# Kernel optimization log

Measured on AMD Instinct MI355X. Metric: run time of the kernel, lower is better.

## Reference

```python
import jax, jax.numpy as jnp
import numpy as np

HEADS = 4
DIM_HEAD = 128
HIDDEN = HEADS * DIM_HEAD  # 512
DIM = 256
EMBED = 256


def mish(x):
    return x * jnp.tanh(jax.nn.softplus(x))


def setup_inputs() -> dict:
    key = jax.random.key(0)
    k = jax.random.split(key, 7)
    b, a, f, t = 64, 8, DIM, 256
    x = jax.random.normal(k[0], (b, a, f, t), dtype=jnp.float32)
    time = jax.random.normal(k[1], (b, a, EMBED), dtype=jnp.float32)
    # to_qkv: Conv2d(dim, 3*hidden, 1, bias=False) -> weight [3*hidden, dim]
    w_qkv = jax.random.normal(k[2], (3 * HIDDEN, DIM), dtype=jnp.float32) * (1.0 / np.sqrt(DIM))
    # time_mlp: Mish -> Linear(embed, 3*hidden)
    w_time = jax.random.normal(k[3], (3 * HIDDEN, EMBED), dtype=jnp.float32) * (1.0 / np.sqrt(EMBED))
    b_time = jax.random.normal(k[4], (3 * HIDDEN,), dtype=jnp.float32) * 0.01
    # to_out: Conv2d(hidden, dim, 1) with bias
    w_out = jax.random.normal(k[5], (DIM, HIDDEN), dtype=jnp.float32) * (1.0 / np.sqrt(HIDDEN))
    b_out = jax.random.normal(k[6], (DIM,), dtype=jnp.float32) * 0.01
    return {"x": x, "time": time, "w_qkv": w_qkv, "w_time": w_time,
            "b_time": b_time, "w_out": w_out, "b_out": b_out}


def reference(x, time, w_qkv, w_time, b_time, w_out, b_out):
    b, a, f, t = x.shape
    heads, c = HEADS, DIM_HEAD
    # x: b a f t -> b f a t (channels-first for 1x1 conv)
    xp = jnp.transpose(x, (0, 2, 1, 3))  # [b, f, a, t]
    # 1x1 conv == channel GEMM
    qkv = jnp.einsum('of,bfat->boat', w_qkv, xp)  # [b, 3*hidden, a, t]
    # time MLP: Mish -> Linear; bias broadcast over t
    temb = mish(time) @ w_time.T + b_time          # [b, a, 3*hidden]
    temb = jnp.transpose(temb, (0, 2, 1))[..., None]  # [b, 3*hidden, a, 1]
    qkv = qkv + temb
    # 'b (qkv heads c) h w -> qkv (b h) heads c w' with h=a, w=t
    qkv = qkv.reshape(b, 3, heads, c, a, t)
    qkv = jnp.transpose(qkv, (1, 0, 4, 2, 3, 5)).reshape(3, b * a, heads, c, t)
    q, k, v = qkv[0], qkv[1], qkv[2]  # each [(b a), heads, c, t]
    k = jax.nn.softmax(k, axis=-1)
    # linear attention: context over keys/values, then apply to q
    context = jnp.einsum('bhdn,bhen->bhde', k, v)   # [(b a), heads, c, c]
    out = jnp.einsum('bhde,bhdn->bhen', context, q)  # [(b a), heads, c, t]
    # '(b h) heads c w -> b (heads c) h w'
    out = out.reshape(b, a, heads * c, t)
    out = jnp.transpose(out, (0, 2, 1, 3))  # [b, hidden, a, t]
    out = jnp.einsum('of,bfat->boat', w_out, out) + b_out[None, :, None, None]
    # b f a t -> b a f t
    return jnp.transpose(out, (0, 2, 1, 3))
```

## Files before the change

kernel.cpp:

```cpp
#include <hip/hip_runtime.h>

typedef __bf16 bf16;
typedef __bf16 bf16x4 __attribute__((ext_vector_type(4)));
typedef __bf16 bf16x8 __attribute__((ext_vector_type(8)));
typedef float  f32x4  __attribute__((ext_vector_type(4)));

#define TT    256
#define FF    256
#define SG    256
#define NGRP  2

#define SCHED0 __builtin_amdgcn_sched_barrier(0)
#define BAR    __builtin_amdgcn_s_barrier()
#define WAITVM(N) asm volatile("s_waitcnt vmcnt(" #N ")" ::: "memory")
#define WAITLGKM0 asm volatile("s_waitcnt lgkmcnt(0)" ::: "memory")

static __device__ inline f32x4 mfma16(bf16x8 a, bf16x8 b, f32x4 c) {
    return __builtin_amdgcn_mfma_f32_16x16x32_bf16(a, b, c, 0, 0, 0);
}

typedef const __attribute__((address_space(1))) unsigned int* gp_t;
typedef __attribute__((address_space(3))) unsigned int* lp_t;
static __device__ inline void gll16(const bf16* g, bf16* l) {
    __builtin_amdgcn_global_load_lds((gp_t)g, (lp_t)l, 16, 0, 0);
}

static __device__ inline void stage128g(const bf16* __restrict__ g, int ld, bf16* __restrict__ l) {
    int lane = threadIdx.x & 63, wv = threadIdx.x >> 6;
    int r = lane >> 2, c8 = (lane & 3) * 8;
#pragma unroll
    for (int i = 0; i < 2; i++) {
        int row0 = wv * 32 + i * 16;
        gll16(g + (size_t)(row0 + r) * ld + c8, l + row0 * 32);
    }
}
static __device__ inline bf16x8 fragld(const bf16* __restrict__ l, int row0) {
    int lane = threadIdx.x & 63;
    return *(const bf16x8*)(l + (row0 + (lane & 15)) * 32 + (lane >> 4) * 8);
}
static __device__ inline bf16x8 fragld_s(const bf16* __restrict__ l, int row0, int stride) {
    int lane = threadIdx.x & 63;
    return *(const bf16x8*)(l + (row0 + (lane & 15)) * stride + (lane >> 4) * 8);
}

__global__ __launch_bounds__(256) void k_cvt(const float4* __restrict__ src, bf16* __restrict__ dst) {
    int i = blockIdx.x * 256 + threadIdx.x;
    float4 v = src[i];
    bf16x4 o;
    o[0] = (__bf16)v.x; o[1] = (__bf16)v.y; o[2] = (__bf16)v.z; o[3] = (__bf16)v.w;
    *(bf16x4*)(dst + (size_t)i * 4) = o;
}

__global__ __launch_bounds__(256) void k_mish(const float4* __restrict__ src, bf16* __restrict__ dst) {
    int i = blockIdx.x * 256 + threadIdx.x;
    float4 v = src[i];
    float in[4] = {v.x, v.y, v.z, v.w};
    bf16x4 o;
#pragma unroll
    for (int j = 0; j < 4; j++) {
        float sp = log1pf(__expf(in[j]));
        o[j] = (__bf16)(in[j] * tanhf(sp));
    }
    *(bf16x4*)(dst + (size_t)i * 4) = o;
}

__global__ __launch_bounds__(256) void k_xpose(const float* __restrict__ x, bf16* __restrict__ xT) {
    __shared__ float tile[64][65];
    int bid = blockIdx.x;
    int s  = bid >> 4;
    int f0 = ((bid >> 2) & 3) * 64;
    int t0 = (bid & 3) * 64;
    int tid = threadIdx.x;
    int rr = tid >> 4;
    int cc = (tid & 15) * 4;
    const float* xp = x + ((size_t)(s * FF + f0)) * TT + t0;
#pragma unroll
    for (int i = 0; i < 4; i++) {
        int r = i * 16 + rr;
        float4 v = *(const float4*)(xp + (size_t)r * TT + cc);
        tile[r][cc] = v.x; tile[r][cc + 1] = v.y; tile[r][cc + 2] = v.z; tile[r][cc + 3] = v.w;
    }
    __syncthreads();
    bf16* op = xT + ((size_t)(s * TT + t0)) * FF + f0;
#pragma unroll
    for (int i = 0; i < 4; i++) {
        int tr = i * 16 + rr;
        bf16x4 o;
        o[0] = (__bf16)tile[cc][tr];     o[1] = (__bf16)tile[cc + 1][tr];
        o[2] = (__bf16)tile[cc + 2][tr]; o[3] = (__bf16)tile[cc + 3][tr];
        *(bf16x4*)(op + (size_t)tr * FF + cc) = o;
    }
}

__global__ __launch_bounds__(256) void k_temb(const bf16* __restrict__ wt, const bf16* __restrict__ mish,
                                              const float* __restrict__ bt, float* __restrict__ tembT) {
    __shared__ bf16 lA[128 * 32];
    __shared__ bf16 lB[128 * 32];
    int o0 = blockIdx.x * 128, s0 = blockIdx.y * 128;
    int tid = threadIdx.x, wv = tid >> 6, lane = tid & 63, qd = lane >> 4, c = lane & 15;
    f32x4 acc[2][8] = {};
    for (int k0 = 0; k0 < 256; k0 += 32) {
        __syncthreads();
        stage128g(wt + (size_t)o0 * 256 + k0, 256, lA);
        stage128g(mish + (size_t)s0 * 256 + k0, 256, lB);
        __syncthreads();
        bf16x8 a0 = fragld(lA, wv * 32), a1 = fragld(lA, wv * 32 + 16);
#pragma unroll
        for (int nt = 0; nt < 8; nt++) {
            bf16x8 b = fragld(lB, nt * 16);
            acc[0][nt] = mfma16(a0, b, acc[0][nt]);
            acc[1][nt] = mfma16(a1, b, acc[1][nt]);
        }
    }
#pragma unroll
    for (int mt = 0; mt < 2; mt++)
#pragma unroll
        for (int nt = 0; nt < 8; nt++)
#pragma unroll
            for (int r = 0; r < 4; r++) {
                int o = o0 + wv * 32 + mt * 16 + qd * 4 + r;
                int s = s0 + nt * 16 + c;
                tembT[(size_t)o * 512 + s] = acc[mt][nt][r] + bt[o];
            }
}

__global__ __launch_bounds__(256) void k_qkv(const bf16* __restrict__ wq, const bf16* __restrict__ xT,
                                             const float* __restrict__ tembT,
                                             bf16* __restrict__ qt, bf16* __restrict__ kk, bf16* __restrict__ vv) {
    __shared__ bf16 lA[2][128 * 32];
    __shared__ bf16 lB[2][128 * 32];
    int b = blockIdx.x;
    int w = (b & 7) * (24 * SG / 8) + (b >> 3);
    int s = w / 24, j = w - s * 24;
    int oc = j >> 1, th = j & 1;
    int o0 = oc * 128, t0 = th * 128;
    int tid = threadIdx.x, wv = tid >> 6, lane = tid & 63, qd = lane >> 4, c = lane & 15;
    const bf16* wA = wq + (size_t)o0 * 256;
    const bf16* xs = xT + (size_t)s * (TT * FF) + (size_t)t0 * FF;
    f32x4 acc[2][8] = {};
    stage128g(wA, 256, lA[0]);
    stage128g(xs, 256, lB[0]);
    SCHED0;
    stage128g(wA + 32, 256, lA[1]);
    stage128g(xs + 32, 256, lB[1]);
    SCHED0;
#pragma unroll
    for (int t = 0; t < 8; t++) {
        if (t == 7) { WAITVM(0); } else { WAITVM(4); }
        SCHED0; BAR; SCHED0;
        bf16x8 a0 = fragld(lA[t & 1], wv * 32), a1 = fragld(lA[t & 1], wv * 32 + 16);
#pragma unroll
        for (int nt = 0; nt < 8; nt++) {
            bf16x8 bfr = fragld(lB[t & 1], nt * 16);
            acc[0][nt] = mfma16(a0, bfr, acc[0][nt]);
            acc[1][nt] = mfma16(a1, bfr, acc[1][nt]);
        }
        SCHED0; BAR; SCHED0;
        if (t + 2 < 8) {
            stage128g(wA + (t + 2) * 32, 256, lA[t & 1]);
            stage128g(xs + (t + 2) * 32, 256, lB[t & 1]);
        }
        SCHED0;
    }
    int sec = oc >> 2, h = oc & 3;
    float tb[2][4];
#pragma unroll
    for (int mt = 0; mt < 2; mt++)
#pragma unroll
        for (int r = 0; r < 4; r++)
            tb[mt][r] = tembT[(size_t)(o0 + wv * 32 + mt * 16 + qd * 4 + r) * 512 + s];
    if (sec == 0) {
#pragma unroll
        for (int mt = 0; mt < 2; mt++)
#pragma unroll
            for (int nt = 0; nt < 8; nt++) {
                int t = t0 + nt * 16 + c, dl = wv * 32 + mt * 16 + qd * 4;
                bf16x4 o;
#pragma unroll
                for (int r = 0; r < 4; r++) o[r] = (__bf16)(acc[mt][nt][r] + tb[mt][r]);
                *(bf16x4*)(qt + (((size_t)s * 4 + h) * 256 + t) * 128 + dl) = o;
            }
    } else {
        bf16* dst0 = (sec == 1 ? kk : vv);
#pragma unroll
        for (int mt = 0; mt < 2; mt++)
#pragma unroll
            for (int nt = 0; nt < 8; nt++) {
                int t = t0 + nt * 16 + c, dl = wv * 32 + mt * 16 + qd * 4;
                bf16* d = dst0 + (((size_t)s * 4 + h) * 128 + dl) * 256 + t;
#pragma unroll
                for (int r = 0; r < 4; r++) d[(size_t)r * 256] = (__bf16)(acc[mt][nt][r] + tb[mt][r]);
            }
    }
}

#define SM_LA2(i) ((bf16*)(smem + 1024 + (size_t)(i) * 8192))
#define SM_LB2(i) ((bf16*)(smem + 1024 + 16384 + (size_t)(i) * 8192))
#define SM_LQ(i)  ((bf16*)(smem + 1024 + (size_t)(i) * 8192))
__global__ __launch_bounds__(256) void k_attn(const bf16* __restrict__ kk, const bf16* __restrict__ vv,
                                              const bf16* __restrict__ qt, bf16* __restrict__ midT) {
    __shared__ __align__(16) char smem[68608];
    float* mx = (float*)smem;
    float* rs = mx + 128;
    bf16* lct = (bf16*)(smem + 1024 + 32768);
    int bid = blockIdx.x;
    int s = bid >> 2, h = bid & 3;
    size_t base = ((size_t)s * 4 + h) * 32768;
    const bf16* kb = kk + base;
    const bf16* vb = vv + base;
    int tid = threadIdx.x, wv = tid >> 6, lane = tid & 63, qd = lane >> 4, c = lane & 15;

    stage128g(vb, 256, SM_LA2(0));
    stage128g(kb, 256, SM_LB2(0));
    SCHED0;
    stage128g(vb + 32, 256, SM_LA2(1));
    stage128g(kb + 32, 256, SM_LB2(1));
    SCHED0;

    {
        int d = tid >> 1, half = tid & 1;
        const bf16* p = kb + (size_t)d * 256 + half * 128;
        float m = -3e38f, l = 0.f;
#pragma unroll
        for (int ci = 0; ci < 16; ci++) {
            bf16x8 v8 = *(const bf16x8*)(p + ci * 8);
            float xv[8]; float cm = -3e38f;
#pragma unroll
            for (int j = 0; j < 8; j++) { xv[j] = (float)v8[j]; cm = fmaxf(cm, xv[j]); }
            if (cm > m) { l *= __expf(m - cm); m = cm; }
#pragma unroll
            for (int j = 0; j < 8; j++) l += __expf(xv[j] - m);
        }
        float mo = __shfl_xor(m, 1);
        float lo = __shfl_xor(l, 1);
        float M = fmaxf(m, mo);
        float L = l * __expf(m - M) + lo * __expf(mo - M);
        if (half == 0) { mx[d] = M; rs[d] = 1.0f / L; }
    }
    __syncthreads();

    f32x4 cacc[2][8] = {};
#pragma unroll
    for (int t = 0; t < 8; t++) {
        if (t == 7) { WAITVM(0); } else { WAITVM(4); }
        SCHED0; BAR; SCHED0;
        bf16x8 a0 = fragld(SM_LA2(t & 1), wv * 32), a1 = fragld(SM_LA2(t & 1), wv * 32 + 16);
#pragma unroll
        for (int nt = 0; nt < 8; nt++) {
            bf16x8 kf = fragld(SM_LB2(t & 1), nt * 16);
            float md = mx[nt * 16 + c];
            bf16x8 bb;
#pragma unroll
            for (int j = 0; j < 8; j++) bb[j] = (__bf16)__expf((float)kf[j] - md);
            cacc[0][nt] = mfma16(a0, bb, cacc[0][nt]);
            cacc[1][nt] = mfma16(a1, bb, cacc[1][nt]);
        }
        SCHED0; BAR; SCHED0;
        if (t + 2 < 8) {
            stage128g(vb + (t + 2) * 32, 256, SM_LA2(t & 1));
            stage128g(kb + (t + 2) * 32, 256, SM_LB2(t & 1));
        }
        SCHED0;
    }

    const bf16* qb = qt + base;
    stage128g(qb, 128, SM_LQ(0));
    SCHED0;
    stage128g(qb + 32, 128, SM_LQ(1));
    SCHED0;

#pragma unroll
    for (int mt = 0; mt < 2; mt++)
#pragma unroll
        for (int nt = 0; nt < 8; nt++) {
            int d = nt * 16 + c;
            float rv = rs[d];
#pragma unroll
            for (int r = 0; r < 4; r++) {
                int e = wv * 32 + mt * 16 + qd * 4 + r;
                lct[e * 136 + d] = (__bf16)(cacc[mt][nt][r] * rv);
            }
        }
    WAITLGKM0;
    SCHED0; BAR; SCHED0;

#pragma unroll
    for (int th = 0; th < 2; th++) {
        f32x4 oacc[2][8] = {};
#pragma unroll
        for (int dd = 0; dd < 4; dd++) {
            int idx = th * 4 + dd;
            int d0 = dd * 32;
            if (idx == 7)                    { WAITVM(0); }
            else if (idx == 4 || idx == 5)   { WAITVM(16); }
            else                             { WAITVM(2); }
            SCHED0; BAR; SCHED0;
            bf16x8 a0 = fragld_s(lct + d0, wv * 32, 136), a1 = fragld_s(lct + d0, wv * 32 + 16, 136);
#pragma unroll
            for (int nt = 0; nt < 8; nt++) {
                bf16x8 qf = fragld(SM_LQ(idx & 1), nt * 16);
                oacc[0][nt] = mfma16(a0, qf, oacc[0][nt]);
                oacc[1][nt] = mfma16(a1, qf, oacc[1][nt]);
            }
            SCHED0; BAR; SCHED0;
            if (idx + 2 < 8) {
                int n = idx + 2;
                stage128g(qb + (size_t)(n >> 2) * 16384 + (n & 3) * 32, 128, SM_LQ(idx & 1));
            }
            SCHED0;
        }
#pragma unroll
        for (int mt = 0; mt < 2; mt++)
#pragma unroll
            for (int nt = 0; nt < 8; nt++) {
                int t = th * 128 + nt * 16 + c;
                int e = wv * 32 + mt * 16 + qd * 4;
                bf16x4 o;
#pragma unroll
                for (int r = 0; r < 4; r++) o[r] = (__bf16)oacc[mt][nt][r];
                *(bf16x4*)(midT + ((size_t)s * 256 + t) * 512 + h * 128 + e) = o;
            }
    }
}

__global__ __launch_bounds__(256) void k_out(const bf16* __restrict__ wo, const bf16* __restrict__ midT,
                                             const float* __restrict__ bo, float* __restrict__ y) {
    __shared__ bf16 lA[2][128 * 32];
    __shared__ bf16 lB[2][128 * 32];
    int b = blockIdx.x;
    int w = (b & 7) * (4 * SG / 8) + (b >> 3);
    int s = w >> 2, j = w & 3;
    int o0 = (j >> 1) * 128, t0 = (j & 1) * 128;
    int tid = threadIdx.x, wv = tid >> 6, lane = tid & 63, qd = lane >> 4, c = lane & 15;
    const bf16* wA = wo + (size_t)o0 * 512;
    const bf16* ms = midT + (size_t)s * 131072 + (size_t)t0 * 512;
    f32x4 acc[2][8] = {};
    stage128g(wA, 512, lA[0]);
    stage128g(ms, 512, lB[0]);
    SCHED0;
    stage128g(wA + 32, 512, lA[1]);
    stage128g(ms + 32, 512, lB[1]);
    SCHED0;
#pragma unroll
    for (int t = 0; t < 16; t++) {
        if (t == 15) { WAITVM(0); } else { WAITVM(4); }
        SCHED0; BAR; SCHED0;
        bf16x8 a0 = fragld(lA[t & 1], wv * 32), a1 = fragld(lA[t & 1], wv * 32 + 16);
#pragma unroll
        for (int nt = 0; nt < 8; nt++) {
            bf16x8 bfr = fragld(lB[t & 1], nt * 16);
            acc[0][nt] = mfma16(a0, bfr, acc[0][nt]);
            acc[1][nt] = mfma16(a1, bfr, acc[1][nt]);
        }
        SCHED0; BAR; SCHED0;
        if (t + 2 < 16) {
            stage128g(wA + (t + 2) * 32, 512, lA[t & 1]);
            stage128g(ms + (t + 2) * 32, 512, lB[t & 1]);
        }
        SCHED0;
    }
    float bb[2][4];
#pragma unroll
    for (int mt = 0; mt < 2; mt++)
#pragma unroll
        for (int r = 0; r < 4; r++)
            bb[mt][r] = bo[o0 + wv * 32 + mt * 16 + qd * 4 + r];
#pragma unroll
    for (int mt = 0; mt < 2; mt++)
#pragma unroll
        for (int nt = 0; nt < 8; nt++)
#pragma unroll
            for (int r = 0; r < 4; r++) {
                int o = o0 + wv * 32 + mt * 16 + qd * 4 + r;
                int t = t0 + nt * 16 + c;
                y[((size_t)(s * 256 + o)) * 256 + t] = acc[mt][nt][r] + bb[mt][r];
            }
}

extern "C" void kernel_launch(void* const* d_in, const int* in_sizes, int n_in,
                              void* d_out, int out_size, void* d_ws, size_t ws_size,
                              hipStream_t stream) {
    const float* x      = (const float*)d_in[0];
    const float* time_  = (const float*)d_in[1];
    const float* w_qkv  = (const float*)d_in[2];
    const float* w_time = (const float*)d_in[3];
    const float* b_time = (const float*)d_in[4];
    const float* w_out  = (const float*)d_in[5];
    const float* b_out  = (const float*)d_in[6];
    float* y = (float*)d_out;
    char* ws = (char*)d_ws;

    bf16*  wqkv_bf  = (bf16*)(ws + 0);
    bf16*  wtime_bf = (bf16*)(ws + 786432);
    bf16*  wout_bf  = (bf16*)(ws + 1572864);
    bf16*  mish_bf  = (bf16*)(ws + 1835008);
    float* tembT    = (float*)(ws + 2097152);
    bf16*  qt       = (bf16*)(ws + 5242880);
    bf16*  kk       = (bf16*)(ws + 72351744);
    bf16*  vv       = (bf16*)(ws + 139460608);
    bf16*  midT     = (bf16*)(ws + 206569472);
    bf16*  xT       = (bf16*)(ws + 206569472);

    k_cvt<<<384, 256, 0, stream>>>((const float4*)w_qkv, wqkv_bf);
    k_cvt<<<384, 256, 0, stream>>>((const float4*)w_time, wtime_bf);
    k_cvt<<<128, 256, 0, stream>>>((const float4*)w_out, wout_bf);
    k_mish<<<128, 256, 0, stream>>>((const float4*)time_, mish_bf);
    k_temb<<<dim3(12, 4), 256, 0, stream>>>(wtime_bf, mish_bf, b_time, tembT);

    for (int g = 0; g < NGRP; g++) {
        const float* xg = x + (size_t)g * SG * FF * TT;
        float*       yg = y + (size_t)g * SG * 256 * TT;
        const float* tg = tembT + (size_t)g * SG;
        k_xpose<<<SG * 16, 256, 0, stream>>>(xg, xT);
        k_qkv<<<24 * SG, 256, 0, stream>>>(wqkv_bf, xT, tg, qt, kk, vv);
        k_attn<<<SG * 4, 256, 0, stream>>>(kk, vv, qt, midT);
        k_out<<<4 * SG, 256, 0, stream>>>(wout_bf, midT, b_out, yg);
    }
}
```

Measured before the change: 616.6 us.

## Stage QKV epilogue through LDS for coalesced 16-byte stores, swap operands for K/V

```diff
diff --git a/kernel.cpp b/kernel.cpp
--- a/kernel.cpp
+++ b/kernel.cpp
@@ -127,70 +127,123 @@
 __global__ __launch_bounds__(256) void k_qkv(const bf16* __restrict__ wq, const bf16* __restrict__ xT,
                                              const float* __restrict__ tembT,
                                              bf16* __restrict__ qt, bf16* __restrict__ kk, bf16* __restrict__ vv) {
-    __shared__ bf16 lA[2][128 * 32];
-    __shared__ bf16 lB[2][128 * 32];
+    __shared__ __align__(16) bf16 sb[4][4096];
+    bf16* sc = &sb[0][0];
     int b = blockIdx.x;
     int w = (b & 7) * (24 * SG / 8) + (b >> 3);
     int s = w / 24, j = w - s * 24;
     int oc = j >> 1, th = j & 1;
     int o0 = oc * 128, t0 = th * 128;
+    int sec = oc >> 2, h = oc & 3;
     int tid = threadIdx.x, wv = tid >> 6, lane = tid & 63, qd = lane >> 4, c = lane & 15;
     const bf16* wA = wq + (size_t)o0 * 256;
     const bf16* xs = xT + (size_t)s * (TT * FF) + (size_t)t0 * FF;
     f32x4 acc[2][8] = {};
-    stage128g(wA, 256, lA[0]);
-    stage128g(xs, 256, lB[0]);
-    SCHED0;
-    stage128g(wA + 32, 256, lA[1]);
-    stage128g(xs + 32, 256, lB[1]);
-    SCHED0;
-#pragma unroll
-    for (int t = 0; t < 8; t++) {
-        if (t == 7) { WAITVM(0); } else { WAITVM(4); }
-        SCHED0; BAR; SCHED0;
-        bf16x8 a0 = fragld(lA[t & 1], wv * 32), a1 = fragld(lA[t & 1], wv * 32 + 16);
-#pragma unroll
-        for (int nt = 0; nt < 8; nt++) {
-            bf16x8 bfr = fragld(lB[t & 1], nt * 16);
-            acc[0][nt] = mfma16(a0, bfr, acc[0][nt]);
-            acc[1][nt] = mfma16(a1, bfr, acc[1][nt]);
-        }
-        SCHED0; BAR; SCHED0;
-        if (t + 2 < 8) {
-            stage128g(wA + (t + 2) * 32, 256, lA[t & 1]);
-            stage128g(xs + (t + 2) * 32, 256, lB[t & 1]);
-        }
-        SCHED0;
-    }
-    int sec = oc >> 2, h = oc & 3;
-    float tb[2][4];
-#pragma unroll
-    for (int mt = 0; mt < 2; mt++)
-#pragma unroll
-        for (int r = 0; r < 4; r++)
-            tb[mt][r] = tembT[(size_t)(o0 + wv * 32 + mt * 16 + qd * 4 + r) * 512 + s];
+    stage128g(wA, 256, sb[0]);
+    stage128g(xs, 256, sb[2]);
+    SCHED0;
+    stage128g(wA + 32, 256, sb[1]);
+    stage128g(xs + 32, 256, sb[3]);
+    SCHED0;
     if (sec == 0) {
 #pragma unroll
+        for (int t = 0; t < 8; t++) {
+            if (t == 7) { WAITVM(0); } else { WAITVM(4); }
+            SCHED0; BAR; SCHED0;
+            bf16x8 a0 = fragld(sb[t & 1], wv * 32), a1 = fragld(sb[t & 1], wv * 32 + 16);
+#pragma unroll
+            for (int nt = 0; nt < 8; nt++) {
+                bf16x8 bfr = fragld(sb[2 + (t & 1)], nt * 16);
+                acc[0][nt] = mfma16(a0, bfr, acc[0][nt]);
+                acc[1][nt] = mfma16(a1, bfr, acc[1][nt]);
+            }
+            SCHED0; BAR; SCHED0;
+            if (t + 2 < 8) {
+                stage128g(wA + (t + 2) * 32, 256, sb[t & 1]);
+                stage128g(xs + (t + 2) * 32, 256, sb[2 + (t & 1)]);
+            }
+            SCHED0;
+        }
+    } else {
+#pragma unroll
+        for (int t = 0; t < 8; t++) {
+            if (t == 7) { WAITVM(0); } else { WAITVM(4); }
+            SCHED0; BAR; SCHED0;
+            bf16x8 a0 = fragld(sb[2 + (t & 1)], wv * 32), a1 = fragld(sb[2 + (t & 1)], wv * 32 + 16);
+#pragma unroll
+            for (int nt = 0; nt < 8; nt++) {
+                bf16x8 bfr = fragld(sb[t & 1], nt * 16);
+                acc[0][nt] = mfma16(a0, bfr, acc[0][nt]);
+                acc[1][nt] = mfma16(a1, bfr, acc[1][nt]);
+            }
+            SCHED0; BAR; SCHED0;
+            if (t + 2 < 8) {
+                stage128g(wA + (t + 2) * 32, 256, sb[t & 1]);
+                stage128g(xs + (t + 2) * 32, 256, sb[2 + (t & 1)]);
+            }
+            SCHED0;
+        }
+    }
+    if (sec == 0) {
+        float tb[2][4];
+#pragma unroll
         for (int mt = 0; mt < 2; mt++)
 #pragma unroll
-            for (int nt = 0; nt < 8; nt++) {
-                int t = t0 + nt * 16 + c, dl = wv * 32 + mt * 16 + qd * 4;
-                bf16x4 o;
-#pragma unroll
-                for (int r = 0; r < 4; r++) o[r] = (__bf16)(acc[mt][nt][r] + tb[mt][r]);
-                *(bf16x4*)(qt + (((size_t)s * 4 + h) * 256 + t) * 128 + dl) = o;
-            }
+            for (int r = 0; r < 4; r++)
+                tb[mt][r] = tembT[(size_t)(o0 + wv * 32 + mt * 16 + qd * 4 + r) * 512 + s];
+        bf16* qbase = qt + (((size_t)s * 4 + h) * 256 + t0) * 128;
+#pragma unroll
+        for (int Ch = 0; Ch < 2; Ch++) {
+#pragma unroll
+            for (int mt = 0; mt < 2; mt++)
+#pragma unroll
+                for (int nt2 = 0; nt2 < 4; nt2++) {
+                    int nt = Ch * 4 + nt2;
+                    int Cl = nt2 * 16 + c;
+                    int dl = wv * 32 + mt * 16 + qd * 4;
+                    bf16x4 o;
+#pragma unroll
+                    for (int r = 0; r < 4; r++) o[r] = (__bf16)(acc[mt][nt][r] + tb[mt][r]);
+                    *(bf16x4*)(sc + Cl * 138 + dl) = o;
+                }
+            WAITLGKM0; SCHED0; BAR; SCHED0;
+#pragma unroll
+            for (int i = 0; i < 4; i++) {
+                int cr = i * 16 + wv * 4 + qd;
+                bf16x8 vrow = *(const bf16x8*)(sc + cr * 138 + c * 8);
+                *(bf16x8*)(qbase + (size_t)(Ch * 64 + cr) * 128 + c * 8) = vrow;
+            }
+            SCHED0; BAR; SCHED0;
+        }
     } else {
-        bf16* dst0 = (sec == 1 ? kk : vv);
-#pragma unroll
-        for (int mt = 0; mt < 2; mt++)
-#pragma unroll
-            for (int nt = 0; nt < 8; nt++) {
-                int t = t0 + nt * 16 + c, dl = wv * 32 + mt * 16 + qd * 4;
-                bf16* d = dst0 + (((size_t)s * 4 + h) * 128 + dl) * 256 + t;
-#pragma unroll
-                for (int r = 0; r < 4; r++) d[(size_t)r * 256] = (__bf16)(acc[mt][nt][r] + tb[mt][r]);
-            }
+        bf16* dst0 = (sec == 1 ? kk : vv) + ((size_t)s * 4 + h) * 32768 + t0;
+        float tb2[8];
+#pragma unroll
+        for (int nt = 0; nt < 8; nt++)
+            tb2[nt] = tembT[(size_t)(o0 + nt * 16 + c) * 512 + s];
+#pragma unroll
+        for (int Ch = 0; Ch < 2; Ch++) {
+#pragma unroll
+            for (int mt = 0; mt < 2; mt++)
+#pragma unroll
+                for (int nt2 = 0; nt2 < 4; nt2++) {
+                    int nt = Ch * 4 + nt2;
+                    int Cl = nt2 * 16 + c;
+                    int tl = wv * 32 + mt * 16 + qd * 4;
+                    bf16x4 o;
+#pragma unroll
+                    for (int r = 0; r < 4; r++) o[r] = (__bf16)(acc[mt][nt][r] + tb2[nt]);
+                    *(bf16x4*)(sc + Cl * 138 + tl) = o;
+                }
+            WAITLGKM0; SCHED0; BAR; SCHED0;
+#pragma unroll
+            for (int i = 0; i < 4; i++) {
+                int cr = i * 16 + wv * 4 + qd;
+                bf16x8 vrow = *(const bf16x8*)(sc + cr * 138 + c * 8);
+                *(bf16x8*)(dst0 + (size_t)(Ch * 64 + cr) * 256 + c * 8) = vrow;
+            }
+            SCHED0; BAR; SCHED0;
+        }
     }
 }
 
```

After: 691.9 us. 1.12x slower.
